# Optimization experiments

Hardware: AMD Instinct MI355X
Metric: run time of the kernel (lower is better)

The kernel has to match this reference:

```python
import jax, jax.numpy as jnp
import numpy as np

NEG_INF = -1e9  # stand-in for -float(config.inf)

def setup_inputs() -> dict:
    key = jax.random.key(0)
    ks = jax.random.split(key, 4)
    B, T, C, H = 8, 2048, 1024, 64
    x = jax.random.normal(ks[0], (B, T, C), dtype=jnp.float32)
    w_k = jax.random.normal(ks[1], (C, H), dtype=jnp.float32) * (C ** -0.5)
    w_q = jax.random.normal(ks[2], (C, H), dtype=jnp.float32) * (C ** -0.5)
    w_v = jax.random.normal(ks[3], (C, H), dtype=jnp.float32) * (C ** -0.5)
    return {"x": x, "w_k": w_k, "w_q": w_q, "w_v": w_v}

def reference(x, w_k, w_q, w_v):
    B, T, C = x.shape
    k = jnp.einsum('btc,ch->bth', x, w_k)  # [B,T,H]
    q = jnp.einsum('btc,ch->bth', x, w_q)
    v = jnp.einsum('btc,ch->bth', x, w_v)
    # NOTE: original scales by C**-0.5 with C = n_emb (not head_size)
    wei = jnp.einsum('bth,bsh->bts', q, k) * (C ** -0.5)  # [B,T,T]
    causal = jnp.tril(jnp.ones((T, T), dtype=bool))
    wei = jnp.where(causal, wei, NEG_INF)
    wei = jax.nn.softmax(wei, axis=-1)
    out = jnp.einsum('bts,bsh->bth', wei, v)  # [B,T,H]
    return out
```

## Files before the change

kernel.cpp:

```cpp
#include <hip/hip_runtime.h>
#include <hip/hip_bf16.h>

#define B_ 8
#define T_ 2048
#define C_ 1024
#define H_ 64

typedef __bf16 bf16x8 __attribute__((ext_vector_type(8)));
typedef float f32x4 __attribute__((ext_vector_type(4)));

__device__ __forceinline__ unsigned short f2bf(float f) {
    union { float f; unsigned u; } v; v.f = f;
    unsigned u = v.u;
    u += 0x7fffu + ((u >> 16) & 1u);
    return (unsigned short)(u >> 16);
}

#define GLOAD16(g, l) __builtin_amdgcn_global_load_lds( \
    (const __attribute__((address_space(1))) void*)(g), \
    (__attribute__((address_space(3))) void*)(l), 16, 0, 0)

#define MFMA16(a, b, c) __builtin_amdgcn_mfma_f32_16x16x32_bf16(a, b, c, 0, 0, 0)

__global__ __launch_bounds__(256) void wtrans_kernel(const float* __restrict__ wk,
                              const float* __restrict__ wq,
                              const float* __restrict__ wv,
                              unsigned short* __restrict__ wt) {
    __shared__ unsigned short ls[64][72];
    const int m = blockIdx.x >> 4, kt = blockIdx.x & 15;
    const float* w = (m == 0) ? wk : (m == 1) ? wq : wv;
    const int tid = threadIdx.x;
    #pragma unroll
    for (int it = 0; it < 4; ++it) {
        int k = it * 16 + (tid >> 4);
        int c = (tid & 15) * 4;
        float4 f = *(const float4*)(w + (size_t)(kt * 64 + k) * 64 + c);
        ls[c][k] = f2bf(f.x); ls[c + 1][k] = f2bf(f.y);
        ls[c + 2][k] = f2bf(f.z); ls[c + 3][k] = f2bf(f.w);
    }
    __syncthreads();
    const int c = tid >> 2, kc = (tid & 3) * 16;
    unsigned short* dst = wt + (size_t)(m * 64 + c) * 1024 + kt * 64 + kc;
    *(uint4*)dst = *(const uint4*)&ls[c][kc];
    *(uint4*)(dst + 8) = *(const uint4*)&ls[c][kc + 8];
}

__global__ __launch_bounds__(256) void qkv_kernel(const float* __restrict__ x,
        const unsigned short* __restrict__ wt,
        unsigned short* __restrict__ kh,
        unsigned short* __restrict__ qh,
        unsigned short* __restrict__ vt) {
    __shared__ __attribute__((aligned(16))) char smem[2][32768];
    const int tid = threadIdx.x;
    const int wid = tid >> 6, lane = tid & 63;
    const int lq = lane & 15, g = lane >> 4;
    const int rg = wid & 1, cg = wid >> 1;
    const int row0 = blockIdx.x * 32;
    const char* xg = (const char*)x;
    const char* wtg = (const char*)wt;

    f32x4 acc[6] = {};

    auto stage = [&](char* buf, int k0) {
        #pragma unroll
        for (int R = 0; R < 2; ++R) {
            int o = R * 4096 + tid * 16;
            int row = o >> 8, inrow = o & 255;
            int src = inrow ^ ((row & 15) << 4);
            GLOAD16(xg + ((size_t)(row0 + row) * 4096 + (size_t)k0 * 4 + src), buf + o);
        }
        #pragma unroll
        for (int R = 0; R < 6; ++R) {
            int o = R * 4096 + tid * 16;
            int row = o >> 7, inrow = o & 127;
            int src = inrow ^ ((row & 7) << 4);
            GLOAD16(wtg + ((size_t)row * 2048 + (size_t)k0 * 2 + src), buf + 8192 + o);
        }
    };

    stage(smem[0], 0);
    asm volatile("s_waitcnt vmcnt(0)" ::: "memory");
    __syncthreads();

    for (int t = 0; t < 16; ++t) {
        char* cur = smem[t & 1];
        if (t < 15) stage(smem[(t + 1) & 1], (t + 1) * 64);

        const char* xb = cur;
        const char* wb = cur + 8192;
        bf16x8 a[2];
        #pragma unroll
        for (int ks = 0; ks < 2; ++ks) {
            int row = rg * 16 + lq;
            int kb0 = ks * 128 + g * 32;
            float4 f0 = *(const float4*)(xb + row * 256 + (kb0 ^ ((row & 15) << 4)));
            float4 f1 = *(const float4*)(xb + row * 256 + ((kb0 + 16) ^ ((row & 15) << 4)));
            union { unsigned short u[8]; bf16x8 v; } u;
            u.u[0] = f2bf(f0.x); u.u[1] = f2bf(f0.y); u.u[2] = f2bf(f0.z); u.u[3] = f2bf(f0.w);
            u.u[4] = f2bf(f1.x); u.u[5] = f2bf(f1.y); u.u[6] = f2bf(f1.z); u.u[7] = f2bf(f1.w);
            a[ks] = u.v;
        }
        #pragma unroll
        for (int j = 0; j < 6; ++j) {
            int row = cg * 96 + j * 16 + lq;
            #pragma unroll
            for (int ks = 0; ks < 2; ++ks) {
                int kb = ks * 64 + g * 16;
                bf16x8 bfrag = *(const bf16x8*)(wb + row * 128 + (kb ^ ((row & 7) << 4)));
                acc[j] = MFMA16(a[ks], bfrag, acc[j]);
            }
        }
        asm volatile("s_waitcnt vmcnt(0)" ::: "memory");
        __syncthreads();
    }

    #pragma unroll
    for (int j = 0; j < 6; ++j) {
        int col = cg * 96 + j * 16 + lq;
        int m = col >> 6, h = col & 63;
        #pragma unroll
        for (int r = 0; r < 4; ++r) {
            int grow = row0 + rg * 16 + g * 4 + r;
            float val = acc[j][r];
            if (m == 0) {
                kh[(size_t)grow * H_ + h] = f2bf(val);
            } else if (m == 1) {
                qh[(size_t)grow * H_ + h] = f2bf(val * 0.03125f);
            } else {
                int bb = grow >> 11, tt = grow & (T_ - 1);
                vt[((size_t)bb * H_ + h) * T_ + tt] = f2bf(val);
            }
        }
    }
}

__global__ __launch_bounds__(256) void attn_kernel(const unsigned short* __restrict__ kh,
        const unsigned short* __restrict__ qh,
        const unsigned short* __restrict__ vt,
        float* __restrict__ out,
        float* __restrict__ po, float* __restrict__ pml, int split) {
    __shared__ __attribute__((aligned(16))) char kv[2][16384];
    __shared__ __attribute__((aligned(16))) char pl[4][2048];
    const int tid = threadIdx.x;
    const int wid = tid >> 6, lane = tid & 63;
    const int lq = lane & 15, g = lane >> 4;

    int b, qt, c, nch;
    if (split) {
        int qtc = blockIdx.x >> 3; b = blockIdx.x & 7;
        qt = 31 - (qtc >> 3); c = qtc & 7;
        nch = (qt + 4) >> 2;
        if (c >= nch) return;
    } else {
        b = blockIdx.x & 7; qt = 31 - (blockIdx.x >> 3); c = 0; nch = 1;
    }
    const int qw = qt * 64 + wid * 16;
    const int q_glob = qw + lq;
    const int s_end_blk = qt * 64 + 64;
    const int sbeg = c << 8;
    const int send = (split && sbeg + 256 < s_end_blk) ? sbeg + 256 : s_end_blk;
    const int nt = (send - sbeg) >> 6;

    const char* khb = (const char*)kh + (size_t)b * T_ * H_ * 2;
    const char* vtb = (const char*)vt + (size_t)b * H_ * T_ * 2;
    const unsigned short* qhb = qh + (size_t)b * T_ * H_;

    bf16x8 qf0 = *(const bf16x8*)(qhb + (qw + lq) * H_ + g * 8);
    bf16x8 qf1 = *(const bf16x8*)(qhb + (qw + lq) * H_ + 32 + g * 8);

    auto stage = [&](char* buf, int s0) {
        #pragma unroll
        for (int R = 0; R < 2; ++R) {
            int o = R * 4096 + wid * 1024;
            int ob = o + lane * 16;
            int row = ob >> 7, inrow = ob & 127;
            int src = inrow ^ ((row & 7) << 4);
            GLOAD16(khb + (size_t)(s0 + row) * 128 + src, buf + o);
        }
        #pragma unroll
        for (int R = 0; R < 2; ++R) {
            int o = R * 4096 + wid * 1024;
            int ob = o + lane * 16;
            int row = ob >> 7, inrow = ob & 127;
            int src = inrow ^ ((row & 7) << 4);
            GLOAD16(vtb + (size_t)row * 4096 + (size_t)s0 * 2 + src, buf + 8192 + o);
        }
    };

    float m_run = -1e30f, l_run = 0.f;
    f32x4 o_acc[4] = {};
    char* pbase = pl[wid];
    const int pswz = (lq & 7) << 4;

    stage(kv[0], sbeg);
    asm volatile("s_waitcnt vmcnt(0)" ::: "memory");
    __syncthreads();

    for (int t = 0; t < nt; ++t) {
        const int s0 = sbeg + t * 64;
        char* cur = kv[t & 1];
        if (t + 1 < nt) stage(kv[(t + 1) & 1], s0 + 64);
        const bool domask = (s0 + 64 == s_end_blk);

        f32x4 sa[4];
        __builtin_amdgcn_s_setprio(1);
        #pragma unroll
        for (int st = 0; st < 4; ++st) {
            int row = st * 16 + lq;
            int swz = (row & 7) << 4;
            f32x4 a = {};
            bf16x8 k0 = *(const bf16x8*)(cur + row * 128 + ((g * 16) ^ swz));
            bf16x8 k1 = *(const bf16x8*)(cur + row * 128 + ((64 + g * 16) ^ swz));
            a = MFMA16(k0, qf0, a);
            a = MFMA16(k1, qf1, a);
            sa[st] = a;
        }
        __builtin_amdgcn_s_setprio(0);

        float p[4][4];
        float smax = -1e30f;
        #pragma unroll
        for (int st = 0; st < 4; ++st)
            #pragma unroll
            for (int r = 0; r < 4; ++r) {
                float v = sa[st][r];
                if (domask) {
                    int sg = s0 + st * 16 + g * 4 + r;
                    v = (sg <= q_glob) ? v : -1e30f;
                }
                p[st][r] = v;
                smax = fmaxf(smax, v);
            }
        smax = fmaxf(smax, __shfl_xor(smax, 16));
        smax = fmaxf(smax, __shfl_xor(smax, 32));
        const float m_new = fmaxf(m_run, smax);
        const float alpha = __expf(m_run - m_new);
        float lsum = 0.f;
        #pragma unroll
        for (int st = 0; st < 4; ++st)
            #pragma unroll
            for (int r = 0; r < 4; ++r) {
                p[st][r] = __expf(p[st][r] - m_new);
                lsum += p[st][r];
            }
        lsum += __shfl_xor(lsum, 16);
        lsum += __shfl_xor(lsum, 32);
        l_run = l_run * alpha + lsum;
        m_run = m_new;
        #pragma unroll
        for (int hc = 0; hc < 4; ++hc) o_acc[hc] *= alpha;

        #pragma unroll
        for (int st = 0; st < 4; ++st) {
            union { unsigned short u[4]; uint2 d; } pk;
            pk.u[0] = f2bf(p[st][0]); pk.u[1] = f2bf(p[st][1]);
            pk.u[2] = f2bf(p[st][2]); pk.u[3] = f2bf(p[st][3]);
            *(uint2*)(pbase + lq * 128 + ((st * 32 + g * 8) ^ pswz)) = pk.d;
        }

        __builtin_amdgcn_s_setprio(1);
        #pragma unroll
        for (int hc = 0; hc < 4; ++hc) {
            int row = hc * 16 + lq;
            int swz = (row & 7) << 4;
            #pragma unroll
            for (int ss = 0; ss < 2; ++ss) {
                bf16x8 vf = *(const bf16x8*)(cur + 8192 + row * 128 + ((ss * 64 + g * 16) ^ swz));
                bf16x8 pb = *(const bf16x8*)(pbase + lq * 128 + ((ss * 64 + g * 16) ^ pswz));
                o_acc[hc] = MFMA16(vf, pb, o_acc[hc]);
            }
        }
        __builtin_amdgcn_s_setprio(0);

        asm volatile("s_waitcnt vmcnt(0)" ::: "memory");
        __syncthreads();
    }

    if (nch == 1) {
        const float inv_l = 1.0f / l_run;
        float* ob = out + ((size_t)b * T_ + qw + lq) * H_;
        #pragma unroll
        for (int hc = 0; hc < 4; ++hc)
            #pragma unroll
            for (int r = 0; r < 4; ++r)
                ob[hc * 16 + g * 4 + r] = o_acc[hc][r] * inv_l;
    } else {
        const int slot = (b * 32 + qt) * 8 + c;
        float* poS = po + (size_t)slot * 4096;
        const int row = wid * 16 + lq;
        #pragma unroll
        for (int hc = 0; hc < 4; ++hc)
            #pragma unroll
            for (int r = 0; r < 4; ++r)
                poS[(size_t)row * 64 + hc * 16 + g * 4 + r] = o_acc[hc][r];
        if (g == 0) {
            pml[slot * 64 + row] = m_run;
            pml[131072 + slot * 64 + row] = l_run;
        }
    }
}

__global__ __launch_bounds__(256) void combine_kernel(const float* __restrict__ po,
        const float* __restrict__ pml, float* __restrict__ out) {
    const int bq = blockIdx.x >> 4, seg = blockIdx.x & 15;
    const int b = bq / 28, qt = 4 + bq % 28;
    const int nch = (qt + 4) >> 2;
    const int r = seg * 4 + (threadIdx.x >> 6);
    const int h = threadIdx.x & 63;
    const int base_slot = (b * 32 + qt) * 8;

    float mv[9], lv[9], ov[9];
    float m = -1e30f;
    #pragma unroll 9
    for (int cc = 0; cc < 9; ++cc) {
        if (cc < nch) {
            mv[cc] = pml[(base_slot + cc) * 64 + r];
            lv[cc] = pml[131072 + (base_slot + cc) * 64 + r];
            ov[cc] = po[(size_t)(base_slot + cc) * 4096 + r * 64 + h];
            m = fmaxf(m, mv[cc]);
        }
    }
    float lsum = 0.f, osum = 0.f;
    #pragma unroll 9
    for (int cc = 0; cc < 9; ++cc) {
        if (cc < nch) {
            float w = __expf(mv[cc] - m);
            lsum += lv[cc] * w;
            osum += ov[cc] * w;
        }
    }
    out[((size_t)b * T_ + qt * 64 + r) * H_ + h] = osum / lsum;
}

extern "C" void kernel_launch(void* const* d_in, const int* in_sizes, int n_in,
                              void* d_out, int out_size, void* d_ws, size_t ws_size,
                              hipStream_t stream) {
    const float* x  = (const float*)d_in[0];
    const float* wk = (const float*)d_in[1];
    const float* wq = (const float*)d_in[2];
    const float* wv = (const float*)d_in[3];
    float* out = (float*)d_out;

    char* ws = (char*)d_ws;
    unsigned short* kh = (unsigned short*)(ws);
    unsigned short* qh = (unsigned short*)(ws + (size_t)2 * 1024 * 1024);
    unsigned short* vt = (unsigned short*)(ws + (size_t)4 * 1024 * 1024);
    unsigned short* wt = (unsigned short*)(ws + (size_t)6 * 1024 * 1024);
    float* po  = (float*)(ws + (size_t)8 * 1024 * 1024);
    float* pml = (float*)(ws + (size_t)40 * 1024 * 1024);

    const bool split = ws_size >= (size_t)42 * 1024 * 1024;

    wtrans_kernel<<<dim3(48), dim3(256), 0, stream>>>(wk, wq, wv, wt);
    qkv_kernel<<<dim3(512), dim3(256), 0, stream>>>(x, wt, kh, qh, vt);
    attn_kernel<<<dim3(split ? 2048 : 256), dim3(256), 0, stream>>>(kh, qh, vt, out, po, pml, split ? 1 : 0);
    if (split)
        combine_kernel<<<dim3(3584), dim3(256), 0, stream>>>(po, pml, out);
}
```

Baseline: 59.97 us.

## Use exp2 softmax with lazy rescaling, bf16 partials, skip final barrier

Folds log2(e) into the Q scale so the softmax can use exp2f, and rescales the running max only when some lane's block max exceeds it by more than 8, which skips the alpha rescale of the accumulators on most tiles. Split-K partial outputs are now stored as bf16 instead of fp32, halving that workspace traffic, and the combine kernel reads them back with exp2. The trailing wait and barrier after the last tile are dropped. The trade-off is lower precision in the partial outputs and possibly larger unnormalized intermediates.

```diff
diff --git a/kernel.cpp b/kernel.cpp
--- a/kernel.cpp
+++ b/kernel.cpp
@@ -15,12 +15,17 @@
     u += 0x7fffu + ((u >> 16) & 1u);
     return (unsigned short)(u >> 16);
 }
+__device__ __forceinline__ float bf2f(unsigned short u) {
+    union { unsigned u; float f; } v; v.u = ((unsigned)u) << 16; return v.f;
+}
 
 #define GLOAD16(g, l) __builtin_amdgcn_global_load_lds( \
     (const __attribute__((address_space(1))) void*)(g), \
     (__attribute__((address_space(3))) void*)(l), 16, 0, 0)
 
 #define MFMA16(a, b, c) __builtin_amdgcn_mfma_f32_16x16x32_bf16(a, b, c, 0, 0, 0)
+
+#define QSCALE 0.04508422003f
 
 __global__ __launch_bounds__(256) void wtrans_kernel(const float* __restrict__ wk,
                               const float* __restrict__ wq,
@@ -125,7 +130,7 @@
             if (m == 0) {
                 kh[(size_t)grow * H_ + h] = f2bf(val);
             } else if (m == 1) {
-                qh[(size_t)grow * H_ + h] = f2bf(val * 0.03125f);
+                qh[(size_t)grow * H_ + h] = f2bf(val * QSCALE);
             } else {
                 int bb = grow >> 11, tt = grow & (T_ - 1);
                 vt[((size_t)bb * H_ + h) * T_ + tt] = f2bf(val);
@@ -138,7 +143,7 @@
         const unsigned short* __restrict__ qh,
         const unsigned short* __restrict__ vt,
         float* __restrict__ out,
-        float* __restrict__ po, float* __restrict__ pml, int split) {
+        unsigned short* __restrict__ po, float* __restrict__ pml, int split) {
     __shared__ __attribute__((aligned(16))) char kv[2][16384];
     __shared__ __attribute__((aligned(16))) char pl[4][2048];
     const int tid = threadIdx.x;
@@ -218,7 +223,7 @@
         __builtin_amdgcn_s_setprio(0);
 
         float p[4][4];
-        float smax = -1e30f;
+        float smax_l = -1e30f;
         #pragma unroll
         for (int st = 0; st < 4; ++st)
             #pragma unroll
@@ -229,26 +234,29 @@
                     v = (sg <= q_glob) ? v : -1e30f;
                 }
                 p[st][r] = v;
-                smax = fmaxf(smax, v);
-            }
-        smax = fmaxf(smax, __shfl_xor(smax, 16));
-        smax = fmaxf(smax, __shfl_xor(smax, 32));
-        const float m_new = fmaxf(m_run, smax);
-        const float alpha = __expf(m_run - m_new);
+                smax_l = fmaxf(smax_l, v);
+            }
+        if (__any(smax_l > m_run + 8.0f)) {
+            float smax = fmaxf(smax_l, __shfl_xor(smax_l, 16));
+            smax = fmaxf(smax, __shfl_xor(smax, 32));
+            float m_new = fmaxf(m_run, smax);
+            float alpha = exp2f(m_run - m_new);
+            l_run *= alpha;
+            #pragma unroll
+            for (int hc = 0; hc < 4; ++hc) o_acc[hc] *= alpha;
+            m_run = m_new;
+        }
         float lsum = 0.f;
         #pragma unroll
         for (int st = 0; st < 4; ++st)
             #pragma unroll
             for (int r = 0; r < 4; ++r) {
-                p[st][r] = __expf(p[st][r] - m_new);
+                p[st][r] = exp2f(p[st][r] - m_run);
                 lsum += p[st][r];
             }
         lsum += __shfl_xor(lsum, 16);
         lsum += __shfl_xor(lsum, 32);
-        l_run = l_run * alpha + lsum;
-        m_run = m_new;
-        #pragma unroll
-        for (int hc = 0; hc < 4; ++hc) o_acc[hc] *= alpha;
+        l_run += lsum;
 
         #pragma unroll
         for (int st = 0; st < 4; ++st) {
@@ -272,8 +280,10 @@
         }
         __builtin_amdgcn_s_setprio(0);
 
-        asm volatile("s_waitcnt vmcnt(0)" ::: "memory");
-        __syncthreads();
+        if (t + 1 < nt) {
+            asm volatile("s_waitcnt vmcnt(0)" ::: "memory");
+            __syncthreads();
+        }
     }
 
     if (nch == 1) {
@@ -286,13 +296,16 @@
                 ob[hc * 16 + g * 4 + r] = o_acc[hc][r] * inv_l;
     } else {
         const int slot = (b * 32 + qt) * 8 + c;
-        float* poS = po + (size_t)slot * 4096;
+        unsigned short* poS = po + (size_t)slot * 4096;
         const int row = wid * 16 + lq;
         #pragma unroll
         for (int hc = 0; hc < 4; ++hc)
             #pragma unroll
-            for (int r = 0; r < 4; ++r)
-                poS[(size_t)row * 64 + hc * 16 + g * 4 + r] = o_acc[hc][r];
+            for (int r = 0; r < 2; ++r) {
+                unsigned lo = f2bf(o_acc[hc][r * 2]);
+                unsigned hi = f2bf(o_acc[hc][r * 2 + 1]);
+                *(unsigned*)(poS + (size_t)row * 64 + hc * 16 + g * 4 + r * 2) = lo | (hi << 16);
+            }
         if (g == 0) {
             pml[slot * 64 + row] = m_run;
             pml[131072 + slot * 64 + row] = l_run;
@@ -300,7 +313,7 @@
     }
 }
 
-__global__ __launch_bounds__(256) void combine_kernel(const float* __restrict__ po,
+__global__ __launch_bounds__(256) void combine_kernel(const unsigned short* __restrict__ po,
         const float* __restrict__ pml, float* __restrict__ out) {
     const int bq = blockIdx.x >> 4, seg = blockIdx.x & 15;
     const int b = bq / 28, qt = 4 + bq % 28;
@@ -316,7 +329,7 @@
         if (cc < nch) {
             mv[cc] = pml[(base_slot + cc) * 64 + r];
             lv[cc] = pml[131072 + (base_slot + cc) * 64 + r];
-            ov[cc] = po[(size_t)(base_slot + cc) * 4096 + r * 64 + h];
+            ov[cc] = bf2f(po[(size_t)(base_slot + cc) * 4096 + r * 64 + h]);
             m = fmaxf(m, mv[cc]);
         }
     }
@@ -324,7 +337,7 @@
     #pragma unroll 9
     for (int cc = 0; cc < 9; ++cc) {
         if (cc < nch) {
-            float w = __expf(mv[cc] - m);
+            float w = exp2f(mv[cc] - m);
             lsum += lv[cc] * w;
             osum += ov[cc] * w;
         }
@@ -346,10 +359,10 @@
     unsigned short* qh = (unsigned short*)(ws + (size_t)2 * 1024 * 1024);
     unsigned short* vt = (unsigned short*)(ws + (size_t)4 * 1024 * 1024);
     unsigned short* wt = (unsigned short*)(ws + (size_t)6 * 1024 * 1024);
-    float* po  = (float*)(ws + (size_t)8 * 1024 * 1024);
-    float* pml = (float*)(ws + (size_t)40 * 1024 * 1024);
-
-    const bool split = ws_size >= (size_t)42 * 1024 * 1024;
+    unsigned short* po = (unsigned short*)(ws + (size_t)8 * 1024 * 1024);
+    float* pml = (float*)(ws + (size_t)24 * 1024 * 1024);
+
+    const bool split = ws_size >= (size_t)25 * 1024 * 1024 + 65536;
 
     wtrans_kernel<<<dim3(48), dim3(256), 0, stream>>>(wk, wq, wv, wt);
     qkv_kernel<<<dim3(512), dim3(256), 0, stream>>>(x, wt, kh, qh, vt);
```

New measurement: 61.16 us. Within noise of the previous version (+2.0%).

## Halve attention KV chunk size and store partial outputs in bf16

Applied to the files above, without the earlier changes.

Split-KV attention now uses 128-key chunks instead of 256, so the grid grows from 2048 to 4096 blocks and work balances better across CUs. Partial outputs are packed as bf16 into a compact triangular slot layout, which cuts workspace writes and combine-kernel reads. The combine kernel merges up to 16 chunks per query tile. In exchange each block does less work (more per-block overhead and more partials to merge), and storing partials in bf16 loses some precision.

```diff
diff --git a/kernel.cpp b/kernel.cpp
--- a/kernel.cpp
+++ b/kernel.cpp
@@ -14,6 +14,13 @@
     unsigned u = v.u;
     u += 0x7fffu + ((u >> 16) & 1u);
     return (unsigned short)(u >> 16);
+}
+__device__ __forceinline__ float bf2f(unsigned short u) {
+    union { unsigned u; float f; } v; v.u = ((unsigned)u) << 16; return v.f;
+}
+__device__ __forceinline__ int cumf(int qt) {
+    int h = qt >> 1;
+    return qt + h * (h - 1) + (qt & 1) * h;
 }
 
 #define GLOAD16(g, l) __builtin_amdgcn_global_load_lds( \
@@ -138,7 +145,7 @@
         const unsigned short* __restrict__ qh,
         const unsigned short* __restrict__ vt,
         float* __restrict__ out,
-        float* __restrict__ po, float* __restrict__ pml, int split) {
+        unsigned short* __restrict__ po, float* __restrict__ pml, int split) {
     __shared__ __attribute__((aligned(16))) char kv[2][16384];
     __shared__ __attribute__((aligned(16))) char pl[4][2048];
     const int tid = threadIdx.x;
@@ -148,8 +155,8 @@
     int b, qt, c, nch;
     if (split) {
         int qtc = blockIdx.x >> 3; b = blockIdx.x & 7;
-        qt = 31 - (qtc >> 3); c = qtc & 7;
-        nch = (qt + 4) >> 2;
+        qt = 31 - (qtc >> 4); c = qtc & 15;
+        nch = (qt + 2) >> 1;
         if (c >= nch) return;
     } else {
         b = blockIdx.x & 7; qt = 31 - (blockIdx.x >> 3); c = 0; nch = 1;
@@ -157,8 +164,8 @@
     const int qw = qt * 64 + wid * 16;
     const int q_glob = qw + lq;
     const int s_end_blk = qt * 64 + 64;
-    const int sbeg = c << 8;
-    const int send = (split && sbeg + 256 < s_end_blk) ? sbeg + 256 : s_end_blk;
+    const int sbeg = c << 7;
+    const int send = (split && sbeg + 128 < s_end_blk) ? sbeg + 128 : s_end_blk;
     const int nt = (send - sbeg) >> 6;
 
     const char* khb = (const char*)kh + (size_t)b * T_ * H_ * 2;
@@ -285,44 +292,48 @@
             for (int r = 0; r < 4; ++r)
                 ob[hc * 16 + g * 4 + r] = o_acc[hc][r] * inv_l;
     } else {
-        const int slot = (b * 32 + qt) * 8 + c;
-        float* poS = po + (size_t)slot * 4096;
+        const int slot = b * 272 + cumf(qt) + c;
+        unsigned short* poS = po + (size_t)slot * 4096;
         const int row = wid * 16 + lq;
         #pragma unroll
         for (int hc = 0; hc < 4; ++hc)
             #pragma unroll
-            for (int r = 0; r < 4; ++r)
-                poS[(size_t)row * 64 + hc * 16 + g * 4 + r] = o_acc[hc][r];
+            for (int r = 0; r < 2; ++r) {
+                unsigned lo = f2bf(o_acc[hc][r * 2]);
+                unsigned hi = f2bf(o_acc[hc][r * 2 + 1]);
+                *(unsigned*)(poS + (size_t)row * 64 + hc * 16 + g * 4 + r * 2) = lo | (hi << 16);
+            }
         if (g == 0) {
             pml[slot * 64 + row] = m_run;
-            pml[131072 + slot * 64 + row] = l_run;
-        }
-    }
-}
-
-__global__ __launch_bounds__(256) void combine_kernel(const float* __restrict__ po,
+            pml[139264 + slot * 64 + row] = l_run;
+        }
+    }
+}
+
+__global__ __launch_bounds__(256) void combine_kernel(const unsigned short* __restrict__ po,
         const float* __restrict__ pml, float* __restrict__ out) {
-    const int bq = blockIdx.x >> 4, seg = blockIdx.x & 15;
-    const int b = bq / 28, qt = 4 + bq % 28;
-    const int nch = (qt + 4) >> 2;
+    const int b = blockIdx.x / 480;
+    const int rem = blockIdx.x % 480;
+    const int qt = 2 + rem / 16, seg = rem % 16;
+    const int nch = (qt + 2) >> 1;
     const int r = seg * 4 + (threadIdx.x >> 6);
     const int h = threadIdx.x & 63;
-    const int base_slot = (b * 32 + qt) * 8;
-
-    float mv[9], lv[9], ov[9];
+    const int base_slot = b * 272 + cumf(qt);
+
+    float mv[16], lv[16], ov[16];
     float m = -1e30f;
-    #pragma unroll 9
-    for (int cc = 0; cc < 9; ++cc) {
+    #pragma unroll 16
+    for (int cc = 0; cc < 16; ++cc) {
         if (cc < nch) {
             mv[cc] = pml[(base_slot + cc) * 64 + r];
-            lv[cc] = pml[131072 + (base_slot + cc) * 64 + r];
-            ov[cc] = po[(size_t)(base_slot + cc) * 4096 + r * 64 + h];
+            lv[cc] = pml[139264 + (base_slot + cc) * 64 + r];
+            ov[cc] = bf2f(po[(size_t)(base_slot + cc) * 4096 + r * 64 + h]);
             m = fmaxf(m, mv[cc]);
         }
     }
     float lsum = 0.f, osum = 0.f;
-    #pragma unroll 9
-    for (int cc = 0; cc < 9; ++cc) {
+    #pragma unroll 16
+    for (int cc = 0; cc < 16; ++cc) {
         if (cc < nch) {
             float w = __expf(mv[cc] - m);
             lsum += lv[cc] * w;
@@ -346,14 +357,14 @@
     unsigned short* qh = (unsigned short*)(ws + (size_t)2 * 1024 * 1024);
     unsigned short* vt = (unsigned short*)(ws + (size_t)4 * 1024 * 1024);
     unsigned short* wt = (unsigned short*)(ws + (size_t)6 * 1024 * 1024);
-    float* po  = (float*)(ws + (size_t)8 * 1024 * 1024);
-    float* pml = (float*)(ws + (size_t)40 * 1024 * 1024);
-
-    const bool split = ws_size >= (size_t)42 * 1024 * 1024;
+    unsigned short* po = (unsigned short*)(ws + (size_t)8 * 1024 * 1024);
+    float* pml = (float*)(ws + (size_t)26 * 1024 * 1024);
+
+    const bool split = ws_size >= (size_t)28 * 1024 * 1024;
 
     wtrans_kernel<<<dim3(48), dim3(256), 0, stream>>>(wk, wq, wv, wt);
     qkv_kernel<<<dim3(512), dim3(256), 0, stream>>>(x, wt, kh, qh, vt);
-    attn_kernel<<<dim3(split ? 2048 : 256), dim3(256), 0, stream>>>(kh, qh, vt, out, po, pml, split ? 1 : 0);
+    attn_kernel<<<dim3(split ? 4096 : 256), dim3(256), 0, stream>>>(kh, qh, vt, out, po, pml, split ? 1 : 0);
     if (split)
-        combine_kernel<<<dim3(3584), dim3(256), 0, stream>>>(po, pml, out);
-}
+        combine_kernel<<<dim3(3840), dim3(256), 0, stream>>>(po, pml, out);
+}
```

Result: slower. 63.78 us (+6.4%).

## Use 32x32 MFMA and 64-row tiles in QKV projection kernel

Applied to the files above, without the earlier changes.

The QKV projection kernel now processes 64 rows per block instead of 32 and switches from 16x16x32 to 32x32x16 bf16 MFMA. Each wave computes a 32x96 output tile with three 16-register accumulators. The aim is to reuse each staged weight tile across twice as many rows, so global and LDS traffic for weights per output drops. The cost is a larger LDS footprint (80KB double buffer), fewer blocks (256 instead of 512), and possibly lower occupancy on a kernel that mostly streams x.

```diff
diff --git a/kernel.cpp b/kernel.cpp
--- a/kernel.cpp
+++ b/kernel.cpp
@@ -8,6 +8,7 @@
 
 typedef __bf16 bf16x8 __attribute__((ext_vector_type(8)));
 typedef float f32x4 __attribute__((ext_vector_type(4)));
+typedef float f32x16 __attribute__((ext_vector_type(16)));
 
 __device__ __forceinline__ unsigned short f2bf(float f) {
     union { float f; unsigned u; } v; v.f = f;
@@ -21,6 +22,7 @@
     (__attribute__((address_space(3))) void*)(l), 16, 0, 0)
 
 #define MFMA16(a, b, c) __builtin_amdgcn_mfma_f32_16x16x32_bf16(a, b, c, 0, 0, 0)
+#define MFMA32(a, b, c) __builtin_amdgcn_mfma_f32_32x32x16_bf16(a, b, c, 0, 0, 0)
 
 __global__ __launch_bounds__(256) void wtrans_kernel(const float* __restrict__ wk,
                               const float* __restrict__ wq,
@@ -50,20 +52,20 @@
         unsigned short* __restrict__ kh,
         unsigned short* __restrict__ qh,
         unsigned short* __restrict__ vt) {
-    __shared__ __attribute__((aligned(16))) char smem[2][32768];
+    __shared__ __attribute__((aligned(16))) char smem[2][40960];
     const int tid = threadIdx.x;
     const int wid = tid >> 6, lane = tid & 63;
-    const int lq = lane & 15, g = lane >> 4;
-    const int rg = wid & 1, cg = wid >> 1;
-    const int row0 = blockIdx.x * 32;
+    const int l31 = lane & 31, hi = lane >> 5;
+    const int rt = wid & 1, cg = wid >> 1;
+    const int row0 = blockIdx.x * 64;
     const char* xg = (const char*)x;
     const char* wtg = (const char*)wt;
 
-    f32x4 acc[6] = {};
+    f32x16 acc[3] = {};
 
     auto stage = [&](char* buf, int k0) {
         #pragma unroll
-        for (int R = 0; R < 2; ++R) {
+        for (int R = 0; R < 4; ++R) {
             int o = R * 4096 + tid * 16;
             int row = o >> 8, inrow = o & 255;
             int src = inrow ^ ((row & 15) << 4);
@@ -74,7 +76,7 @@
             int o = R * 4096 + tid * 16;
             int row = o >> 7, inrow = o & 127;
             int src = inrow ^ ((row & 7) << 4);
-            GLOAD16(wtg + ((size_t)row * 2048 + (size_t)k0 * 2 + src), buf + 8192 + o);
+            GLOAD16(wtg + ((size_t)row * 2048 + (size_t)k0 * 2 + src), buf + 16384 + o);
         }
     };
 
@@ -82,32 +84,34 @@
     asm volatile("s_waitcnt vmcnt(0)" ::: "memory");
     __syncthreads();
 
+    const int arow = rt * 32 + l31;
+    const int aswz = (arow & 15) << 4;
+
     for (int t = 0; t < 16; ++t) {
         char* cur = smem[t & 1];
         if (t < 15) stage(smem[(t + 1) & 1], (t + 1) * 64);
 
         const char* xb = cur;
-        const char* wb = cur + 8192;
-        bf16x8 a[2];
-        #pragma unroll
-        for (int ks = 0; ks < 2; ++ks) {
-            int row = rg * 16 + lq;
-            int kb0 = ks * 128 + g * 32;
-            float4 f0 = *(const float4*)(xb + row * 256 + (kb0 ^ ((row & 15) << 4)));
-            float4 f1 = *(const float4*)(xb + row * 256 + ((kb0 + 16) ^ ((row & 15) << 4)));
+        const char* wb = cur + 16384;
+        bf16x8 a4[4];
+        #pragma unroll
+        for (int f = 0; f < 4; ++f) {
+            int off = f * 64 + hi * 32;
+            float4 f0 = *(const float4*)(xb + arow * 256 + (off ^ aswz));
+            float4 f1 = *(const float4*)(xb + arow * 256 + ((off + 16) ^ aswz));
             union { unsigned short u[8]; bf16x8 v; } u;
             u.u[0] = f2bf(f0.x); u.u[1] = f2bf(f0.y); u.u[2] = f2bf(f0.z); u.u[3] = f2bf(f0.w);
             u.u[4] = f2bf(f1.x); u.u[5] = f2bf(f1.y); u.u[6] = f2bf(f1.z); u.u[7] = f2bf(f1.w);
-            a[ks] = u.v;
-        }
-        #pragma unroll
-        for (int j = 0; j < 6; ++j) {
-            int row = cg * 96 + j * 16 + lq;
-            #pragma unroll
-            for (int ks = 0; ks < 2; ++ks) {
-                int kb = ks * 64 + g * 16;
-                bf16x8 bfrag = *(const bf16x8*)(wb + row * 128 + (kb ^ ((row & 7) << 4)));
-                acc[j] = MFMA16(a[ks], bfrag, acc[j]);
+            a4[f] = u.v;
+        }
+        #pragma unroll
+        for (int ct = 0; ct < 3; ++ct) {
+            int brow = cg * 96 + ct * 32 + l31;
+            int bswz = (brow & 7) << 4;
+            #pragma unroll
+            for (int f = 0; f < 4; ++f) {
+                bf16x8 b = *(const bf16x8*)(wb + brow * 128 + ((f * 32 + hi * 16) ^ bswz));
+                acc[ct] = MFMA32(a4[f], b, acc[ct]);
             }
         }
         asm volatile("s_waitcnt vmcnt(0)" ::: "memory");
@@ -115,13 +119,13 @@
     }
 
     #pragma unroll
-    for (int j = 0; j < 6; ++j) {
-        int col = cg * 96 + j * 16 + lq;
+    for (int ct = 0; ct < 3; ++ct) {
+        int col = cg * 96 + ct * 32 + l31;
         int m = col >> 6, h = col & 63;
         #pragma unroll
-        for (int r = 0; r < 4; ++r) {
-            int grow = row0 + rg * 16 + g * 4 + r;
-            float val = acc[j][r];
+        for (int reg = 0; reg < 16; ++reg) {
+            int grow = row0 + rt * 32 + (reg & 3) + 8 * (reg >> 2) + 4 * hi;
+            float val = acc[ct][reg];
             if (m == 0) {
                 kh[(size_t)grow * H_ + h] = f2bf(val);
             } else if (m == 1) {
@@ -352,7 +356,7 @@
     const bool split = ws_size >= (size_t)42 * 1024 * 1024;
 
     wtrans_kernel<<<dim3(48), dim3(256), 0, stream>>>(wk, wq, wv, wt);
-    qkv_kernel<<<dim3(512), dim3(256), 0, stream>>>(x, wt, kh, qh, vt);
+    qkv_kernel<<<dim3(256), dim3(256), 0, stream>>>(x, wt, kh, qh, vt);
     attn_kernel<<<dim3(split ? 2048 : 256), dim3(256), 0, stream>>>(kh, qh, vt, out, po, pml, split ? 1 : 0);
     if (split)
         combine_kernel<<<dim3(3584), dim3(256), 0, stream>>>(po, pml, out);
```

Result: slower. 66.28 us (+10.5%).
